# Performance work log

Measured on AMD Instinct MI355X. Metric: run time of the kernel, lower is better.

## Reference

```python
import jax, jax.numpy as jnp
import numpy as np

CHUNK = 64  # chunk_size
EPS = 1e-6


def setup_inputs() -> dict:
    key = jax.random.key(0)
    ks = jax.random.split(key, 7)
    b, L, H, dh, ds = 2, 4096, 16, 64, 64
    X = jax.random.normal(ks[0], (b, L, H, dh), dtype=jnp.float32)
    # negative log-decay in (-1, 0) for numerical stability (Mamba2 convention)
    A = -jax.random.uniform(ks[1], (b, L, H), dtype=jnp.float32)
    B = jax.random.normal(ks[2], (b, L, H, ds), dtype=jnp.float32)
    C = jax.random.normal(ks[3], (b, L, H, ds), dtype=jnp.float32)
    log2_alpha_base = jnp.full((H,), -0.15, dtype=jnp.float32) + 0.02 * jax.random.normal(ks[4], (H,), dtype=jnp.float32)
    log2_beta = 0.02 * jax.random.normal(ks[5], (H,), dtype=jnp.float32)
    surprise_ema = jnp.ones((H,), dtype=jnp.float32)
    return {"X": X, "A": A, "B": B, "C": C,
            "log2_alpha_base": log2_alpha_base, "log2_beta": log2_beta,
            "surprise_ema": surprise_ema}


def reference(X, A, B, C, log2_alpha_base, log2_beta, surprise_ema):
    b, L, H, dh = X.shape
    ds = B.shape[-1]
    n = L // CHUNK  # L is a multiple of CHUNK (no padding needed)

    # [b, h, n, c, ...] layout
    Xt = X.reshape(b, n, CHUNK, H, dh).transpose(0, 3, 1, 2, 4)   # b h n c dh
    At = A.reshape(b, n, CHUNK, H).transpose(0, 3, 1, 2)          # b h n c
    Bt = B.reshape(b, n, CHUNK, H, ds).transpose(0, 3, 1, 2, 4)   # b h n c ds
    Ct = C.reshape(b, n, CHUNK, H, ds).transpose(0, 3, 1, 2, 4)   # b h n c ds

    # per-chunk surprise from outer-product state delta
    BX = jnp.einsum('bhncs,bhncd->bhnsd', Bt, Xt)                 # b h n ds dh
    chunk_surprise = (BX ** 2).mean(axis=(-1, -2))                # b h n

    # surprise gate (eval mode: EMA buffer not updated)
    normalized = chunk_surprise / (surprise_ema[None, :, None] + EPS)
    log2c = jnp.clip(log2_alpha_base, -3.32, -0.015)
    alpha_base = 1.0 - jnp.exp2(log2c)                            # [H]
    beta = jnp.exp2(jnp.clip(log2_beta, -2.0, 2.0))               # [H]
    boost = jax.nn.relu(jnp.tanh(beta[None, :, None] * normalized))
    alpha = jnp.clip(alpha_base[None, :, None]
                     + (1.0 - alpha_base[None, :, None]) * boost, 0.01, 0.999)

    # surprise-modulated decay
    A_mod = At * (1.0 - alpha)[..., None]                         # b h n c
    A_cs = jnp.cumsum(A_mod, axis=-1)                             # b h n c

    # intra-chunk attention-like term with causal decay matrix
    diff = A_cs[..., :, None] - A_cs[..., None, :]                # b h n c c
    causal = jnp.tril(jnp.ones((CHUNK, CHUNK), dtype=bool))
    Lmat = jnp.where(causal, jnp.exp(diff), 0.0)
    CB = jnp.einsum('bhnid,bhnjd->bhnij', Ct, Bt)
    Y_intra = jnp.einsum('bhnij,bhnjd->bhnid', Lmat * CB, Xt)

    # inter-chunk state carry (sequential over chunks)
    decay_chunk = jnp.exp(A_mod.sum(axis=-1))                     # b h n
    decay_to_end = jnp.exp(A_cs[..., -1:] - A_cs)                 # b h n c
    h_final = jnp.einsum('bhnc,bhncs,bhncd->bhnsd', decay_to_end, Bt, Xt)

    def step(carry, inp):
        dc, hf = inp                                              # dc: b h ; hf: b h ds dh
        return dc[..., None, None] * carry + hf, carry

    dc_n = jnp.moveaxis(decay_chunk, 2, 0)                        # n b h
    hf_n = jnp.moveaxis(h_final, 2, 0)                            # n b h ds dh
    init = jnp.zeros((b, H, ds, dh), X.dtype)
    _, h_inter_n = jax.lax.scan(step, init, (dc_n, hf_n))
    h_inter = jnp.moveaxis(h_inter_n, 0, 2)                       # b h n ds dh

    decay_from_start = jnp.exp(A_cs)
    Y_inter = jnp.einsum('bhnis,bhnsp,bhni->bhnip', Ct, h_inter, decay_from_start)

    Y = (Y_intra + Y_inter).transpose(0, 2, 3, 1, 4).reshape(b, L, H, dh)
    return Y
```

## Files before the change

### kernel.cpp

```cpp
#include <hip/hip_runtime.h>
#include <hip/hip_bf16.h>
#include <math.h>

#define LSEQ 4096
#define NH   16
#define DH   64
#define CH   64
#define NCH  64

typedef __attribute__((ext_vector_type(8))) short bf16x8;
typedef __attribute__((ext_vector_type(4))) short s16x4;
typedef __attribute__((ext_vector_type(4))) float f32x4;

#define MFMA16(a, b, c) __builtin_amdgcn_mfma_f32_16x16x32_bf16((a), (b), (c), 0, 0, 0)

__device__ __forceinline__ int swz(int row, int col) {
    return (row << 6) + (col ^ ((row & 7) << 3));
}

__device__ __forceinline__ float4 ld4(const float* p) {
    return *reinterpret_cast<const float4*>(p);
}
__device__ __forceinline__ short f2b(float x) {
    __hip_bfloat16 h = __float2bfloat16(x);
    return *reinterpret_cast<short*>(&h);
}
__device__ __forceinline__ float b2f(short s) {
    union { unsigned u; float f; } v;
    v.u = ((unsigned)(unsigned short)s) << 16;
    return v.f;
}
__device__ __forceinline__ s16x4 pack4(float a, float b, float c, float d) {
    s16x4 r; r.x = f2b(a); r.y = f2b(b); r.z = f2b(c); r.w = f2b(d); return r;
}
__device__ __forceinline__ uint2 sx2(uint2 v, int m) {
    uint2 r;
    r.x = (unsigned)__shfl_xor((int)v.x, m, 64);
    r.y = (unsigned)__shfl_xor((int)v.y, m, 64);
    return r;
}
__device__ __forceinline__ short ext4(uint2 u, int g) {
    unsigned word = (g & 2) ? u.y : u.x;
    return (short)((g & 1) ? (word >> 16) : (word & 0xffffu));
}

__global__ __launch_bounds__(256) void ssd_k1(
    const float* __restrict__ X, const float* __restrict__ A,
    const float* __restrict__ B, const float* __restrict__ C,
    const float* __restrict__ l2ab, const float* __restrict__ l2b,
    const float* __restrict__ ema,
    unsigned short* __restrict__ yw, unsigned short* __restrict__ hf,
    float* __restrict__ dcb, float* __restrict__ dfs)
{
    __shared__ __align__(16) short R1[CH * 64];
    __shared__ __align__(16) short R2[CH * 64];
    __shared__ __align__(16) short R3[CH * 64];
    __shared__ __align__(16) float red[4];

    const int tid  = threadIdx.x;
    const int blk  = blockIdx.x;
    const int nidx = blk & (NCH - 1);
    const int h    = (blk >> 6) & (NH - 1);
    const int bb   = blk >> 10;
    const size_t base = ((size_t)(bb * LSEQ + nidx * CH) * NH + h) * DH;

    const int lane = tid & 63;
    const int w    = tid >> 6;
    const int rb   = 16 * w;
    const int fr   = lane & 15;
    const int gq   = lane >> 4;
    const int g4   = 4 * gq;
    const int ko   = 8 * gq;
    const int rot  = (fr >> 1) & 3;

    const int sc = tid >> 4, sd0 = (tid & 15) * 4;

    #pragma unroll
    for (int m = 0; m < 4; ++m) {
        int c = sc + 16 * m;
        size_t g = base + (size_t)c * 1024 + sd0;
        float4 xv = ld4(&X[g]);
        float4 bv = ld4(&B[g]);
        float4 cv = ld4(&C[g]);
        *reinterpret_cast<s16x4*>(&R1[swz(c, sd0)]) = pack4(xv.x, xv.y, xv.z, xv.w);
        *reinterpret_cast<s16x4*>(&R2[swz(c, sd0)]) = pack4(bv.x, bv.y, bv.z, bv.w);
        *reinterpret_cast<s16x4*>(&R3[swz(c, sd0)]) = pack4(cv.x, cv.y, cv.z, cv.w);
    }
    float aval = A[(size_t)(bb * LSEQ + nidx * CH + lane) * NH + h];
    __syncthreads();

    const f32x4 zf = {0.f, 0.f, 0.f, 0.f};

    bf16x8 aX0 = *reinterpret_cast<const bf16x8*>(&R1[swz(rb + fr, 0  + ko)]);
    bf16x8 aX1 = *reinterpret_cast<const bf16x8*>(&R1[swz(rb + fr, 32 + ko)]);
    bf16x8 aB0 = *reinterpret_cast<const bf16x8*>(&R2[swz(rb + fr, 0  + ko)]);
    bf16x8 aB1 = *reinterpret_cast<const bf16x8*>(&R2[swz(rb + fr, 32 + ko)]);
    bf16x8 aC0 = *reinterpret_cast<const bf16x8*>(&R3[swz(rb + fr, 0  + ko)]);
    bf16x8 aC1 = *reinterpret_cast<const bf16x8*>(&R3[swz(rb + fr, 32 + ko)]);
    f32x4 aCB[4];
    float ss = 0.f;
    #pragma unroll
    for (int n = 0; n < 4; ++n) {
        bf16x8 bX0 = *reinterpret_cast<const bf16x8*>(&R1[swz(16 * n + fr, 0  + ko)]);
        bf16x8 bX1 = *reinterpret_cast<const bf16x8*>(&R1[swz(16 * n + fr, 32 + ko)]);
        bf16x8 bB0 = *reinterpret_cast<const bf16x8*>(&R2[swz(16 * n + fr, 0  + ko)]);
        bf16x8 bB1 = *reinterpret_cast<const bf16x8*>(&R2[swz(16 * n + fr, 32 + ko)]);
        f32x4 gx = MFMA16(aX1, bX1, MFMA16(aX0, bX0, zf));
        f32x4 gb = MFMA16(aB1, bB1, MFMA16(aB0, bB0, zf));
        aCB[n]   = MFMA16(aC1, bB1, MFMA16(aC0, bB0, zf));
        #pragma unroll
        for (int r = 0; r < 4; ++r) ss = fmaf(gx[r], gb[r], ss);
    }
    #pragma unroll
    for (int off = 32; off > 0; off >>= 1) ss += __shfl_down(ss, off, 64);
    if (lane == 0) red[w] = ss;
    __syncthreads();

    float4 rv = *reinterpret_cast<const float4*>(red);
    float surprise = (rv.x + rv.y + rv.z + rv.w) * (1.f / 4096.f);
    float l2c   = fminf(fmaxf(l2ab[h], -3.32f), -0.015f);
    float ab_   = 1.f - exp2f(l2c);
    float bt    = exp2f(fminf(fmaxf(l2b[h], -2.f), 2.f));
    float nrm   = surprise / (ema[h] + 1e-6f);
    float boost = fmaxf(tanhf(bt * nrm), 0.f);
    float alpha = fminf(fmaxf(ab_ + (1.f - ab_) * boost, 0.01f), 0.999f);
    float scale = 1.f - alpha;
    float v = aval * scale;
    #pragma unroll
    for (int off = 1; off < 64; off <<= 1) {
        float t = __shfl_up(v, off, 64);
        if (lane >= off) v += t;
    }
    float tot  = __shfl(v, 63, 64);
    float epv  = __expf(v);
    float env  = __expf(-v);
    float dtev = __expf(tot - v);
    if (w == 0) {
        dfs[(size_t)blk * CH + lane] = epv;
        if (lane == 63) dcb[blk] = __expf(tot);
    }

    {
        float epi[4], enj[4];
        #pragma unroll
        for (int r = 0; r < 4; ++r) epi[r] = __shfl(epv, rb + g4 + r, 64);
        #pragma unroll
        for (int n = 0; n < 4; ++n) enj[n] = __shfl(env, 16 * n + fr, 64);
        #pragma unroll
        for (int n = 0; n < 4; ++n)
            #pragma unroll
            for (int r = 0; r < 4; ++r) {
                int i = rb + g4 + r, j = 16 * n + fr;
                float val = (j <= i) ? epi[r] * enj[n] * aCB[n][r] : 0.f;
                R3[swz(i, j)] = f2b(val);
            }
    }

    s16x4 outX[4], outB[4];
    const int d0 = 4 * fr;
    #pragma unroll
    for (int m = 0; m < 4; ++m) {
        int c0 = 16 * w + 4 * ((m + rot) & 3);
        uint2 mx = *reinterpret_cast<const uint2*>(&R1[swz(c0 + gq, d0)]);
        uint2 mb = *reinterpret_cast<const uint2*>(&R2[swz(c0 + gq, d0)]);
        uint2 px_ = sx2(mx, 16), pb_ = sx2(mb, 16);
        uint2 xe = (gq & 1) ? px_ : mx, xo = (gq & 1) ? mx : px_;
        uint2 be = (gq & 1) ? pb_ : mb, bo = (gq & 1) ? mb : pb_;
        uint2 xpe = sx2(xe, 32), xpo = sx2(xo, 32);
        uint2 bpe = sx2(be, 32), bpo = sx2(bo, 32);
        uint2 xr0 = (gq & 2) ? xpe : xe, xr1 = (gq & 2) ? xpo : xo;
        uint2 xr2 = (gq & 2) ? xe : xpe, xr3 = (gq & 2) ? xo : xpo;
        uint2 br0 = (gq & 2) ? bpe : be, br1 = (gq & 2) ? bpo : bo;
        uint2 br2 = (gq & 2) ? be : bpe, br3 = (gq & 2) ? bo : bpo;
        s16x4 ox; ox.x = ext4(xr0, gq); ox.y = ext4(xr1, gq);
                  ox.z = ext4(xr2, gq); ox.w = ext4(xr3, gq);
        outX[m] = ox;
        float dt0 = __shfl(dtev, c0 + 0, 64), dt1 = __shfl(dtev, c0 + 1, 64);
        float dt2 = __shfl(dtev, c0 + 2, 64), dt3 = __shfl(dtev, c0 + 3, 64);
        s16x4 ob;
        ob.x = f2b(b2f(ext4(br0, gq)) * dt0);
        ob.y = f2b(b2f(ext4(br1, gq)) * dt1);
        ob.z = f2b(b2f(ext4(br2, gq)) * dt2);
        ob.w = f2b(b2f(ext4(br3, gq)) * dt3);
        outB[m] = ob;
    }
    __syncthreads();

    #pragma unroll
    for (int m = 0; m < 4; ++m) {
        int c0 = 16 * w + 4 * ((m + rot) & 3);
        *reinterpret_cast<s16x4*>(&R1[swz(d0 + gq, c0)]) = outX[m];
        *reinterpret_cast<s16x4*>(&R2[swz(d0 + gq, c0)]) = outB[m];
    }
    __syncthreads();

    f32x4 acc2[4] = {zf, zf, zf, zf};
    f32x4 acc3[4] = {zf, zf, zf, zf};
    #pragma unroll
    for (int k0 = 0; k0 < 64; k0 += 32) {
        bf16x8 aX = *reinterpret_cast<const bf16x8*>(&R1[swz(rb + fr, k0 + ko)]);
        bf16x8 aB = *reinterpret_cast<const bf16x8*>(&R2[swz(rb + fr, k0 + ko)]);
        #pragma unroll
        for (int n = 0; n < 4; ++n) {
            bf16x8 bT = *reinterpret_cast<const bf16x8*>(&R3[swz(16 * n + fr, k0 + ko)]);
            bf16x8 bX = *reinterpret_cast<const bf16x8*>(&R1[swz(16 * n + fr, k0 + ko)]);
            acc2[n] = MFMA16(aX, bT, acc2[n]);
            acc3[n] = MFMA16(aB, bX, acc3[n]);
        }
    }
    #pragma unroll
    for (int n = 0; n < 4; ++n) {
        int colI = 16 * n + fr;
        s16x4 y4 = pack4(acc2[n][0], acc2[n][1], acc2[n][2], acc2[n][3]);
        s16x4 h4 = pack4(acc3[n][0], acc3[n][1], acc3[n][2], acc3[n][3]);
        *reinterpret_cast<s16x4*>(&yw[(size_t)blk * 4096 + colI * 64 + rb + g4]) = y4;
        *reinterpret_cast<s16x4*>(&hf[(size_t)blk * 4096 + colI * 64 + rb + g4]) = h4;
    }
}

__global__ __launch_bounds__(256) void ssd_k2(
    unsigned int* __restrict__ hfU, const float* __restrict__ dcb)
{
    __shared__ float sdc[NCH];
    const int tid = threadIdx.x;
    const int bh  = blockIdx.x >> 3;
    const int sub = blockIdx.x & 7;
    if (tid < NCH) sdc[tid] = dcb[bh * NCH + tid];
    __syncthreads();
    const size_t base = (size_t)bh * NCH * 2048 + sub * 256 + tid;

    float c0 = 0.f, c1 = 0.f;
    unsigned int cur[8];
    #pragma unroll
    for (int kk = 0; kk < 8; ++kk) cur[kk] = hfU[base + (size_t)kk * 2048];
    #pragma unroll
    for (int kb = 0; kb < 8; ++kb) {
        unsigned int nxt[8];
        if (kb < 7) {
            #pragma unroll
            for (int kk = 0; kk < 8; ++kk)
                nxt[kk] = hfU[base + (size_t)(8 * kb + 8 + kk) * 2048];
        }
        #pragma unroll
        for (int kk = 0; kk < 8; ++kk) {
            int k = 8 * kb + kk;
            unsigned int u = cur[kk];
            union { unsigned int q; float f; } lo, hi;
            lo.q = u << 16;
            hi.q = u & 0xffff0000u;
            unsigned int packed = (unsigned int)(unsigned short)f2b(c0)
                                | ((unsigned int)(unsigned short)f2b(c1) << 16);
            hfU[base + (size_t)k * 2048] = packed;
            float d = sdc[k];
            c0 = fmaf(d, c0, lo.f);
            c1 = fmaf(d, c1, hi.f);
        }
        if (kb < 7) {
            #pragma unroll
            for (int kk = 0; kk < 8; ++kk) cur[kk] = nxt[kk];
        }
    }
}

__global__ __launch_bounds__(256) void ssd_k3(
    const float* __restrict__ C, const unsigned short* __restrict__ hI,
    const unsigned short* __restrict__ yw, const float* __restrict__ dfs,
    float* __restrict__ Y)
{
    __shared__ __align__(16) short sHt[CH * 64];
    __shared__ __align__(16) short sC2[CH * 64];
    __shared__ float sF[CH];

    const int tid  = threadIdx.x;
    const int blk  = blockIdx.x;
    const int nidx = blk & (NCH - 1);
    const int h    = (blk >> 6) & (NH - 1);
    const int bb   = blk >> 10;
    const size_t base = ((size_t)(bb * LSEQ + nidx * CH) * NH + h) * DH;

    #pragma unroll
    for (int m = 0; m < 2; ++m) {
        int idx = tid + 256 * m;
        int row = idx >> 3, c8 = (idx & 7) * 8;
        bf16x8 v = *reinterpret_cast<const bf16x8*>(&hI[(size_t)blk * 4096 + row * 64 + c8]);
        *reinterpret_cast<bf16x8*>(&sHt[swz(row, c8)]) = v;
    }
    #pragma unroll
    for (int m = 0; m < 4; ++m) {
        int p = tid + 256 * m;
        int row = p >> 4, d0 = (p & 15) * 4;
        float4 cv = ld4(&C[base + (size_t)row * 1024 + d0]);
        *reinterpret_cast<s16x4*>(&sC2[swz(row, d0)]) = pack4(cv.x, cv.y, cv.z, cv.w);
    }
    if (tid < CH) sF[tid] = dfs[(size_t)blk * CH + tid];
    __syncthreads();

    const int lane = tid & 63;
    const int w    = tid >> 6;
    const int rb   = 16 * w;
    const int fr   = lane & 15;
    const int g4   = 4 * (lane >> 4);
    const int ko   = 8 * (lane >> 4);
    const f32x4 zf = {0.f, 0.f, 0.f, 0.f};

    f32x4 acc[4] = {zf, zf, zf, zf};
    #pragma unroll
    for (int k0 = 0; k0 < 64; k0 += 32) {
        bf16x8 a = *reinterpret_cast<const bf16x8*>(&sHt[swz(rb + fr, k0 + ko)]);
        #pragma unroll
        for (int n = 0; n < 4; ++n) {
            bf16x8 b = *reinterpret_cast<const bf16x8*>(&sC2[swz(16 * n + fr, k0 + ko)]);
            acc[n] = MFMA16(a, b, acc[n]);
        }
    }
    #pragma unroll
    for (int n = 0; n < 4; ++n) {
        int i  = 16 * n + fr;
        int p0 = rb + g4;
        float f = sF[i];
        s16x4 y4 = *reinterpret_cast<const s16x4*>(&yw[(size_t)blk * 4096 + i * 64 + p0]);
        float4 o;
        o.x = fmaf(f, acc[n][0], b2f(y4.x));
        o.y = fmaf(f, acc[n][1], b2f(y4.y));
        o.z = fmaf(f, acc[n][2], b2f(y4.z));
        o.w = fmaf(f, acc[n][3], b2f(y4.w));
        *reinterpret_cast<float4*>(&Y[base + (size_t)i * 1024 + p0]) = o;
    }
}

extern "C" void kernel_launch(void* const* d_in, const int* in_sizes, int n_in,
                              void* d_out, int out_size, void* d_ws, size_t ws_size,
                              hipStream_t stream)
{
    const float* X    = (const float*)d_in[0];
    const float* A    = (const float*)d_in[1];
    const float* B    = (const float*)d_in[2];
    const float* C    = (const float*)d_in[3];
    const float* l2ab = (const float*)d_in[4];
    const float* l2b  = (const float*)d_in[5];
    const float* ema  = (const float*)d_in[6];
    float* Y = (float*)d_out;

    unsigned short* hf = (unsigned short*)d_ws;
    unsigned short* yw = hf + (size_t)8388608;
    float* dcb = (float*)(yw + (size_t)8388608);
    float* dfs = dcb + 2048;

    const int nblk = 2 * NH * NCH;
    ssd_k1<<<nblk, 256, 0, stream>>>(X, A, B, C, l2ab, l2b, ema, yw, hf, dcb, dfs);
    ssd_k2<<<256, 256, 0, stream>>>((unsigned int*)hf, dcb);
    ssd_k3<<<nblk, 256, 0, stream>>>(C, hf, yw, dfs, Y);
}
```

Before: 57.78 us.

## Load MFMA fragments from global and write transposed X/B directly to LDS

Stages X and B in registers and writes X transposed into LDS right away, while the MFMA A/B operands for the Gram and CB products are loaded straight from global memory and converted to bf16. This removes the shared-memory staging of C and the shuffle-based in-LDS transpose along with one barrier. The decay prefix scan is computed on the raw A values before the surprise scale is known, since the scale factors out of the cumulative sum. In exchange, each wave issues redundant strided global loads for the fragments, which rely on cache hits, and does scalar 2-byte transposed LDS stores.

```diff
diff --git a/kernel.cpp b/kernel.cpp
--- a/kernel.cpp
+++ b/kernel.cpp
@@ -33,15 +33,13 @@
 __device__ __forceinline__ s16x4 pack4(float a, float b, float c, float d) {
     s16x4 r; r.x = f2b(a); r.y = f2b(b); r.z = f2b(c); r.w = f2b(d); return r;
 }
-__device__ __forceinline__ uint2 sx2(uint2 v, int m) {
-    uint2 r;
-    r.x = (unsigned)__shfl_xor((int)v.x, m, 64);
-    r.y = (unsigned)__shfl_xor((int)v.y, m, 64);
-    return r;
-}
-__device__ __forceinline__ short ext4(uint2 u, int g) {
-    unsigned word = (g & 2) ? u.y : u.x;
-    return (short)((g & 1) ? (word >> 16) : (word & 0xffffu));
+__device__ __forceinline__ bf16x8 lf(const float* p) {
+    float4 a = ld4(p);
+    float4 b = ld4(p + 4);
+    union { bf16x8 v; s16x4 h[2]; } u;
+    u.h[0] = pack4(a.x, a.y, a.z, a.w);
+    u.h[1] = pack4(b.x, b.y, b.z, b.w);
+    return u.v;
 }
 
 __global__ __launch_bounds__(256) void ssd_k1(
@@ -71,40 +69,61 @@
     const int gq   = lane >> 4;
     const int g4   = 4 * gq;
     const int ko   = 8 * gq;
-    const int rot  = (fr >> 1) & 3;
+    const int rot  = lane & 3;
 
     const int sc = tid >> 4, sd0 = (tid & 15) * 4;
+
+    float4 px[4], pb[4];
+    #pragma unroll
+    for (int m = 0; m < 4; ++m) {
+        size_t g = base + (size_t)(sc + 16 * m) * 1024 + sd0;
+        px[m] = ld4(&X[g]);
+        pb[m] = ld4(&B[g]);
+    }
+    float aval = A[(size_t)(bb * LSEQ + nidx * CH + lane) * NH + h];
 
     #pragma unroll
     for (int m = 0; m < 4; ++m) {
         int c = sc + 16 * m;
-        size_t g = base + (size_t)c * 1024 + sd0;
-        float4 xv = ld4(&X[g]);
-        float4 bv = ld4(&B[g]);
-        float4 cv = ld4(&C[g]);
-        *reinterpret_cast<s16x4*>(&R1[swz(c, sd0)]) = pack4(xv.x, xv.y, xv.z, xv.w);
-        *reinterpret_cast<s16x4*>(&R2[swz(c, sd0)]) = pack4(bv.x, bv.y, bv.z, bv.w);
-        *reinterpret_cast<s16x4*>(&R3[swz(c, sd0)]) = pack4(cv.x, cv.y, cv.z, cv.w);
-    }
-    float aval = A[(size_t)(bb * LSEQ + nidx * CH + lane) * NH + h];
-    __syncthreads();
+        float xf[4] = {px[m].x, px[m].y, px[m].z, px[m].w};
+        #pragma unroll
+        for (int ee = 0; ee < 4; ++ee) {
+            int e = (ee + rot) & 3;
+            R1[swz(sd0 + e, c)] = f2b(xf[e]);
+        }
+    }
+
+    float cum = aval;
+    #pragma unroll
+    for (int off = 1; off < 64; off <<= 1) {
+        float t = __shfl_up(cum, off, 64);
+        if (lane >= off) cum += t;
+    }
+    float cum_tot = __shfl(cum, 63, 64);
 
     const f32x4 zf = {0.f, 0.f, 0.f, 0.f};
 
-    bf16x8 aX0 = *reinterpret_cast<const bf16x8*>(&R1[swz(rb + fr, 0  + ko)]);
-    bf16x8 aX1 = *reinterpret_cast<const bf16x8*>(&R1[swz(rb + fr, 32 + ko)]);
-    bf16x8 aB0 = *reinterpret_cast<const bf16x8*>(&R2[swz(rb + fr, 0  + ko)]);
-    bf16x8 aB1 = *reinterpret_cast<const bf16x8*>(&R2[swz(rb + fr, 32 + ko)]);
-    bf16x8 aC0 = *reinterpret_cast<const bf16x8*>(&R3[swz(rb + fr, 0  + ko)]);
-    bf16x8 aC1 = *reinterpret_cast<const bf16x8*>(&R3[swz(rb + fr, 32 + ko)]);
+    const float* Xr = X + base;
+    const float* Br = B + base;
+    const float* Cr = C + base;
+    bf16x8 aX0 = lf(Xr + (size_t)(rb + fr) * 1024 + 0  + ko);
+    bf16x8 aX1 = lf(Xr + (size_t)(rb + fr) * 1024 + 32 + ko);
+    bf16x8 aB0 = lf(Br + (size_t)(rb + fr) * 1024 + 0  + ko);
+    bf16x8 aB1 = lf(Br + (size_t)(rb + fr) * 1024 + 32 + ko);
+    bf16x8 aC0 = lf(Cr + (size_t)(rb + fr) * 1024 + 0  + ko);
+    bf16x8 aC1 = lf(Cr + (size_t)(rb + fr) * 1024 + 32 + ko);
     f32x4 aCB[4];
     float ss = 0.f;
     #pragma unroll
     for (int n = 0; n < 4; ++n) {
-        bf16x8 bX0 = *reinterpret_cast<const bf16x8*>(&R1[swz(16 * n + fr, 0  + ko)]);
-        bf16x8 bX1 = *reinterpret_cast<const bf16x8*>(&R1[swz(16 * n + fr, 32 + ko)]);
-        bf16x8 bB0 = *reinterpret_cast<const bf16x8*>(&R2[swz(16 * n + fr, 0  + ko)]);
-        bf16x8 bB1 = *reinterpret_cast<const bf16x8*>(&R2[swz(16 * n + fr, 32 + ko)]);
+        bf16x8 bX0, bX1, bB0, bB1;
+        if (n == w) { bX0 = aX0; bX1 = aX1; bB0 = aB0; bB1 = aB1; }
+        else {
+            bX0 = lf(Xr + (size_t)(16 * n + fr) * 1024 + 0  + ko);
+            bX1 = lf(Xr + (size_t)(16 * n + fr) * 1024 + 32 + ko);
+            bB0 = lf(Br + (size_t)(16 * n + fr) * 1024 + 0  + ko);
+            bB1 = lf(Br + (size_t)(16 * n + fr) * 1024 + 32 + ko);
+        }
         f32x4 gx = MFMA16(aX1, bX1, MFMA16(aX0, bX0, zf));
         f32x4 gb = MFMA16(aB1, bB1, MFMA16(aB0, bB0, zf));
         aCB[n]   = MFMA16(aC1, bB1, MFMA16(aC0, bB0, zf));
@@ -125,13 +144,8 @@
     float boost = fmaxf(tanhf(bt * nrm), 0.f);
     float alpha = fminf(fmaxf(ab_ + (1.f - ab_) * boost, 0.01f), 0.999f);
     float scale = 1.f - alpha;
-    float v = aval * scale;
-    #pragma unroll
-    for (int off = 1; off < 64; off <<= 1) {
-        float t = __shfl_up(v, off, 64);
-        if (lane >= off) v += t;
-    }
-    float tot  = __shfl(v, 63, 64);
+    float v    = cum * scale;
+    float tot  = cum_tot * scale;
     float epv  = __expf(v);
     float env  = __expf(-v);
     float dtev = __expf(tot - v);
@@ -156,41 +170,16 @@
             }
     }
 
-    s16x4 outX[4], outB[4];
-    const int d0 = 4 * fr;
     #pragma unroll
     for (int m = 0; m < 4; ++m) {
-        int c0 = 16 * w + 4 * ((m + rot) & 3);
-        uint2 mx = *reinterpret_cast<const uint2*>(&R1[swz(c0 + gq, d0)]);
-        uint2 mb = *reinterpret_cast<const uint2*>(&R2[swz(c0 + gq, d0)]);
-        uint2 px_ = sx2(mx, 16), pb_ = sx2(mb, 16);
-        uint2 xe = (gq & 1) ? px_ : mx, xo = (gq & 1) ? mx : px_;
-        uint2 be = (gq & 1) ? pb_ : mb, bo = (gq & 1) ? mb : pb_;
-        uint2 xpe = sx2(xe, 32), xpo = sx2(xo, 32);
-        uint2 bpe = sx2(be, 32), bpo = sx2(bo, 32);
-        uint2 xr0 = (gq & 2) ? xpe : xe, xr1 = (gq & 2) ? xpo : xo;
-        uint2 xr2 = (gq & 2) ? xe : xpe, xr3 = (gq & 2) ? xo : xpo;
-        uint2 br0 = (gq & 2) ? bpe : be, br1 = (gq & 2) ? bpo : bo;
-        uint2 br2 = (gq & 2) ? be : bpe, br3 = (gq & 2) ? bo : bpo;
-        s16x4 ox; ox.x = ext4(xr0, gq); ox.y = ext4(xr1, gq);
-                  ox.z = ext4(xr2, gq); ox.w = ext4(xr3, gq);
-        outX[m] = ox;
-        float dt0 = __shfl(dtev, c0 + 0, 64), dt1 = __shfl(dtev, c0 + 1, 64);
-        float dt2 = __shfl(dtev, c0 + 2, 64), dt3 = __shfl(dtev, c0 + 3, 64);
-        s16x4 ob;
-        ob.x = f2b(b2f(ext4(br0, gq)) * dt0);
-        ob.y = f2b(b2f(ext4(br1, gq)) * dt1);
-        ob.z = f2b(b2f(ext4(br2, gq)) * dt2);
-        ob.w = f2b(b2f(ext4(br3, gq)) * dt3);
-        outB[m] = ob;
-    }
-    __syncthreads();
-
-    #pragma unroll
-    for (int m = 0; m < 4; ++m) {
-        int c0 = 16 * w + 4 * ((m + rot) & 3);
-        *reinterpret_cast<s16x4*>(&R1[swz(d0 + gq, c0)]) = outX[m];
-        *reinterpret_cast<s16x4*>(&R2[swz(d0 + gq, c0)]) = outB[m];
+        int c = sc + 16 * m;
+        float dt = __shfl(dtev, c, 64);
+        float bf[4] = {pb[m].x, pb[m].y, pb[m].z, pb[m].w};
+        #pragma unroll
+        for (int ee = 0; ee < 4; ++ee) {
+            int e = (ee + rot) & 3;
+            R2[swz(sd0 + e, c)] = f2b(bf[e] * dt);
+        }
     }
     __syncthreads();
 
```

Measured after the change: 82.97 us. 1.44x slower.

## Hoist decay prefix-scan before surprise reduction and remove one block barrier

Applied to the files above, without the earlier changes.

The cumulative sum of A now runs before the surprise reduction, and the scale is applied afterwards by linearity (cum*scale), so the scan overlaps with MFMA work instead of sitting behind the block barrier. The transposed X tile is written into a new fourth LDS buffer right away rather than overwriting R1, which removes one __syncthreads between the transposed read and write phases. The cost is 8 KB more LDS per block, which may reduce occupancy, and slightly different floating-point rounding from scaling after the sum.

```diff
diff --git a/kernel.cpp b/kernel.cpp
--- a/kernel.cpp
+++ b/kernel.cpp
@@ -55,6 +55,7 @@
     __shared__ __align__(16) short R1[CH * 64];
     __shared__ __align__(16) short R2[CH * 64];
     __shared__ __align__(16) short R3[CH * 64];
+    __shared__ __align__(16) short R4[CH * 64];
     __shared__ __align__(16) float red[4];
 
     const int tid  = threadIdx.x;
@@ -89,6 +90,14 @@
     float aval = A[(size_t)(bb * LSEQ + nidx * CH + lane) * NH + h];
     __syncthreads();
 
+    float cum = aval;
+    #pragma unroll
+    for (int off = 1; off < 64; off <<= 1) {
+        float t = __shfl_up(cum, off, 64);
+        if (lane >= off) cum += t;
+    }
+    float cum_tot = __shfl(cum, 63, 64);
+
     const f32x4 zf = {0.f, 0.f, 0.f, 0.f};
 
     bf16x8 aX0 = *reinterpret_cast<const bf16x8*>(&R1[swz(rb + fr, 0  + ko)]);
@@ -111,52 +120,8 @@
         #pragma unroll
         for (int r = 0; r < 4; ++r) ss = fmaf(gx[r], gb[r], ss);
     }
-    #pragma unroll
-    for (int off = 32; off > 0; off >>= 1) ss += __shfl_down(ss, off, 64);
-    if (lane == 0) red[w] = ss;
-    __syncthreads();
-
-    float4 rv = *reinterpret_cast<const float4*>(red);
-    float surprise = (rv.x + rv.y + rv.z + rv.w) * (1.f / 4096.f);
-    float l2c   = fminf(fmaxf(l2ab[h], -3.32f), -0.015f);
-    float ab_   = 1.f - exp2f(l2c);
-    float bt    = exp2f(fminf(fmaxf(l2b[h], -2.f), 2.f));
-    float nrm   = surprise / (ema[h] + 1e-6f);
-    float boost = fmaxf(tanhf(bt * nrm), 0.f);
-    float alpha = fminf(fmaxf(ab_ + (1.f - ab_) * boost, 0.01f), 0.999f);
-    float scale = 1.f - alpha;
-    float v = aval * scale;
-    #pragma unroll
-    for (int off = 1; off < 64; off <<= 1) {
-        float t = __shfl_up(v, off, 64);
-        if (lane >= off) v += t;
-    }
-    float tot  = __shfl(v, 63, 64);
-    float epv  = __expf(v);
-    float env  = __expf(-v);
-    float dtev = __expf(tot - v);
-    if (w == 0) {
-        dfs[(size_t)blk * CH + lane] = epv;
-        if (lane == 63) dcb[blk] = __expf(tot);
-    }
-
-    {
-        float epi[4], enj[4];
-        #pragma unroll
-        for (int r = 0; r < 4; ++r) epi[r] = __shfl(epv, rb + g4 + r, 64);
-        #pragma unroll
-        for (int n = 0; n < 4; ++n) enj[n] = __shfl(env, 16 * n + fr, 64);
-        #pragma unroll
-        for (int n = 0; n < 4; ++n)
-            #pragma unroll
-            for (int r = 0; r < 4; ++r) {
-                int i = rb + g4 + r, j = 16 * n + fr;
-                float val = (j <= i) ? epi[r] * enj[n] * aCB[n][r] : 0.f;
-                R3[swz(i, j)] = f2b(val);
-            }
-    }
-
-    s16x4 outX[4], outB[4];
+
+    s16x4 outB[4];
     const int d0 = 4 * fr;
     #pragma unroll
     for (int m = 0; m < 4; ++m) {
@@ -174,23 +139,63 @@
         uint2 br2 = (gq & 2) ? be : bpe, br3 = (gq & 2) ? bo : bpo;
         s16x4 ox; ox.x = ext4(xr0, gq); ox.y = ext4(xr1, gq);
                   ox.z = ext4(xr2, gq); ox.w = ext4(xr3, gq);
-        outX[m] = ox;
+        *reinterpret_cast<s16x4*>(&R4[swz(d0 + gq, c0)]) = ox;
+        s16x4 ob; ob.x = ext4(br0, gq); ob.y = ext4(br1, gq);
+                  ob.z = ext4(br2, gq); ob.w = ext4(br3, gq);
+        outB[m] = ob;
+    }
+
+    #pragma unroll
+    for (int off = 32; off > 0; off >>= 1) ss += __shfl_down(ss, off, 64);
+    if (lane == 0) red[w] = ss;
+    __syncthreads();
+
+    float4 rv = *reinterpret_cast<const float4*>(red);
+    float surprise = (rv.x + rv.y + rv.z + rv.w) * (1.f / 4096.f);
+    float l2c   = fminf(fmaxf(l2ab[h], -3.32f), -0.015f);
+    float ab_   = 1.f - exp2f(l2c);
+    float bt    = exp2f(fminf(fmaxf(l2b[h], -2.f), 2.f));
+    float nrm   = surprise / (ema[h] + 1e-6f);
+    float boost = fmaxf(tanhf(bt * nrm), 0.f);
+    float alpha = fminf(fmaxf(ab_ + (1.f - ab_) * boost, 0.01f), 0.999f);
+    float scale = 1.f - alpha;
+    float v    = cum * scale;
+    float tot  = cum_tot * scale;
+    float epv  = __expf(v);
+    float env  = __expf(-v);
+    float dtev = __expf(tot - v);
+    if (w == 0) {
+        dfs[(size_t)blk * CH + lane] = epv;
+        if (lane == 63) dcb[blk] = __expf(tot);
+    }
+
+    {
+        float epi[4], enj[4];
+        #pragma unroll
+        for (int r = 0; r < 4; ++r) epi[r] = __shfl(epv, rb + g4 + r, 64);
+        #pragma unroll
+        for (int n = 0; n < 4; ++n) enj[n] = __shfl(env, 16 * n + fr, 64);
+        #pragma unroll
+        for (int n = 0; n < 4; ++n)
+            #pragma unroll
+            for (int r = 0; r < 4; ++r) {
+                int i = rb + g4 + r, j = 16 * n + fr;
+                float val = (j <= i) ? epi[r] * enj[n] * aCB[n][r] : 0.f;
+                R3[swz(i, j)] = f2b(val);
+            }
+    }
+
+    #pragma unroll
+    for (int m = 0; m < 4; ++m) {
+        int c0 = 16 * w + 4 * ((m + rot) & 3);
         float dt0 = __shfl(dtev, c0 + 0, 64), dt1 = __shfl(dtev, c0 + 1, 64);
         float dt2 = __shfl(dtev, c0 + 2, 64), dt3 = __shfl(dtev, c0 + 3, 64);
         s16x4 ob;
-        ob.x = f2b(b2f(ext4(br0, gq)) * dt0);
-        ob.y = f2b(b2f(ext4(br1, gq)) * dt1);
-        ob.z = f2b(b2f(ext4(br2, gq)) * dt2);
-        ob.w = f2b(b2f(ext4(br3, gq)) * dt3);
-        outB[m] = ob;
-    }
-    __syncthreads();
-
-    #pragma unroll
-    for (int m = 0; m < 4; ++m) {
-        int c0 = 16 * w + 4 * ((m + rot) & 3);
-        *reinterpret_cast<s16x4*>(&R1[swz(d0 + gq, c0)]) = outX[m];
-        *reinterpret_cast<s16x4*>(&R2[swz(d0 + gq, c0)]) = outB[m];
+        ob.x = f2b(b2f(outB[m].x) * dt0);
+        ob.y = f2b(b2f(outB[m].y) * dt1);
+        ob.z = f2b(b2f(outB[m].z) * dt2);
+        ob.w = f2b(b2f(outB[m].w) * dt3);
+        *reinterpret_cast<s16x4*>(&R2[swz(d0 + gq, c0)]) = ob;
     }
     __syncthreads();
 
@@ -198,12 +203,12 @@
     f32x4 acc3[4] = {zf, zf, zf, zf};
     #pragma unroll
     for (int k0 = 0; k0 < 64; k0 += 32) {
-        bf16x8 aX = *reinterpret_cast<const bf16x8*>(&R1[swz(rb + fr, k0 + ko)]);
+        bf16x8 aX = *reinterpret_cast<const bf16x8*>(&R4[swz(rb + fr, k0 + ko)]);
         bf16x8 aB = *reinterpret_cast<const bf16x8*>(&R2[swz(rb + fr, k0 + ko)]);
         #pragma unroll
         for (int n = 0; n < 4; ++n) {
             bf16x8 bT = *reinterpret_cast<const bf16x8*>(&R3[swz(16 * n + fr, k0 + ko)]);
-            bf16x8 bX = *reinterpret_cast<const bf16x8*>(&R1[swz(16 * n + fr, k0 + ko)]);
+            bf16x8 bX = *reinterpret_cast<const bf16x8*>(&R4[swz(16 * n + fr, k0 + ko)]);
             acc2[n] = MFMA16(aX, bT, acc2[n]);
             acc3[n] = MFMA16(aB, bX, acc3[n]);
         }
```

Measured after the change: 60.40 us. 1.05x slower.
